# Optimization experiments

Hardware: AMD Instinct MI355X
Metric: run time of the kernel (lower is better)

## Reference

```python
import jax, jax.numpy as jnp
import numpy as np

B, N, D = 64, 512, 128  # graphs per batch, max nodes per graph, hidden_dim


def setup_inputs() -> dict:
    key = jax.random.key(0)
    ks = jax.random.split(key, 9)
    h1 = jax.random.normal(ks[0], (B, N, D), jnp.float32)
    h2 = jax.random.normal(ks[1], (B, N, D), jnp.float32)
    s = 1.0 / np.sqrt(D)
    Wk = jax.random.normal(ks[2], (D, D), jnp.float32) * s
    bk = jax.random.normal(ks[3], (D,), jnp.float32) * s
    Wq = jax.random.normal(ks[4], (D, D), jnp.float32) * s
    bq = jax.random.normal(ks[5], (D,), jnp.float32) * s
    t = jnp.asarray(np.sqrt(1.0 / D), jnp.float32)  # self.t = sqrt(1/hidden_dim)
    len1 = jax.random.randint(ks[6], (B,), 1, N + 1, jnp.int32)
    len2 = jax.random.randint(ks[7], (B,), 1, N + 1, jnp.int32)
    return {"h1": h1, "h2": h2, "Wk": Wk, "bk": bk, "Wq": Wq, "bq": bq,
            "t": t, "len1": len1, "len2": len2}


def reference(h1, h2, Wk, bk, Wq, bq, t, len1, len2):
    # valid-node masks for the ragged (padded) graphs
    pos = jnp.arange(N)
    m1 = pos[None, :] < len1[:, None]  # [B, N]
    m2 = pos[None, :] < len2[:, None]  # [B, N]

    # k = Linear(h), q = Linear(h)  (torch Linear: x @ W.T + b)
    k1 = jnp.einsum('bnd,ed->bne', h1, Wk) + bk
    k2 = jnp.einsum('bnd,ed->bne', h2, Wk) + bk
    q1 = jnp.einsum('bnd,ed->bne', h1, Wq) + bq
    q2 = jnp.einsum('bnd,ed->bne', h2, Wq) + bq

    NEG = jnp.asarray(-1e9, h1.dtype)

    # g1 nodes attend over g2 nodes; note values == keys (k2)
    s1 = jnp.einsum('bnd,bmd->bnm', q1, k2) * t           # [B, N1, N2]
    s1 = jnp.where(m2[:, None, :], s1, NEG)
    a1 = jax.nn.softmax(s1, axis=-1)
    o1 = jnp.einsum('bnm,bmd->bnd', a1, k2) * m1[:, :, None]

    # g2 nodes attend over g1 nodes; values == k1
    s2 = jnp.einsum('bnd,bmd->bnm', q2, k1) * t           # [B, N2, N1]
    s2 = jnp.where(m1[:, None, :], s2, NEG)
    a2 = jax.nn.softmax(s2, axis=-1)
    o2 = jnp.einsum('bnm,bmd->bnd', a2, k1) * m2[:, :, None]

    return o1, o2
```

## Files before the change

### kernel.cpp

```cpp
#include <hip/hip_runtime.h>

typedef __attribute__((ext_vector_type(8))) short bf16x8;
typedef __attribute__((ext_vector_type(4))) short s16x4;
typedef __attribute__((ext_vector_type(4))) float f32x4;
typedef __attribute__((ext_vector_type(4))) int   i32x4;

#define MFMA16 __builtin_amdgcn_mfma_f32_16x16x32_bf16

#define B_ 64
#define N_ 512
#define D_ 128
#define BUFB 16384

__device__ __forceinline__ unsigned short f2bf(float f) {
  unsigned u = __builtin_bit_cast(unsigned, f);
  u += 0x7fffu + ((u >> 16) & 1u);
  return (unsigned short)(u >> 16);
}
__device__ __forceinline__ int packbf2(float lo, float hi) {
  return (int)((unsigned)f2bf(lo) | ((unsigned)f2bf(hi) << 16));
}

__device__ __forceinline__ void gload_lds16(const void* g, void* l) {
  __builtin_amdgcn_global_load_lds((const __attribute__((address_space(1))) unsigned*)g,
                                   (__attribute__((address_space(3))) unsigned*)l, 16, 0, 0);
}

__global__ void prep_w(const float* __restrict__ Wk, const float* __restrict__ Wq,
                       const float* __restrict__ bq, const float* __restrict__ tptr,
                       short* __restrict__ wkb, short* __restrict__ wqb,
                       float* __restrict__ bqs) {
  const float sc = tptr[0] * 1.4426950408889634f;
  int i = blockIdx.x * 256 + threadIdx.x;
  if (i < D_ * D_) { wkb[i] = (short)f2bf(Wk[i]); wqb[i] = (short)f2bf(Wq[i] * sc); }
  if (i < D_) bqs[i] = bq[i] * sc;
}

__global__ __launch_bounds__(256, 2) void proj_kernel(
    const float* __restrict__ h1, const float* __restrict__ h2,
    const short* __restrict__ wkb, const short* __restrict__ wqb,
    const float* __restrict__ bk, const float* __restrict__ bqs,
    short* __restrict__ k1, short* __restrict__ k2,
    short* __restrict__ q1, short* __restrict__ q2,
    short* __restrict__ k1T, short* __restrict__ k2T) {
  const int wave = threadIdx.x >> 6, lane = threadIdx.x & 63;
  const int c = lane & 15, g = lane >> 4;
  const int rw = blockIdx.x * 128 + wave * 32;
  const int inp = rw >> 15;
  const int loc = rw & 32767;
  const int b = loc >> 9, n0 = loc & 511;
  const float* __restrict__ h = inp ? h2 : h1;
  short* __restrict__ kout = inp ? k2 : k1;
  short* __restrict__ qout = inp ? q2 : q1;
  short* __restrict__ kT   = inp ? k2T : k1T;

  bf16x8 xf[2][4];
#pragma unroll
  for (int mt = 0; mt < 2; ++mt) {
    const float* hr = h + (long)(loc + mt * 16 + c) * D_;
#pragma unroll
    for (int kk = 0; kk < 4; ++kk) {
      f32x4 lo = *(const f32x4*)(hr + kk * 32 + g * 8);
      f32x4 hi = *(const f32x4*)(hr + kk * 32 + g * 8 + 4);
      bf16x8 v;
      v[0] = (short)f2bf(lo[0]); v[1] = (short)f2bf(lo[1]);
      v[2] = (short)f2bf(lo[2]); v[3] = (short)f2bf(lo[3]);
      v[4] = (short)f2bf(hi[0]); v[5] = (short)f2bf(hi[1]);
      v[6] = (short)f2bf(hi[2]); v[7] = (short)f2bf(hi[3]);
      xf[mt][kk] = v;
    }
  }

#pragma unroll
  for (int et = 0; et < 8; ++et) {
    bf16x8 wkf[4], wqf[4];
    const short* wkr = wkb + (et * 16 + c) * D_;
    const short* wqr = wqb + (et * 16 + c) * D_;
#pragma unroll
    for (int kk = 0; kk < 4; ++kk) {
      wkf[kk] = *(const bf16x8*)(wkr + kk * 32 + g * 8);
      wqf[kk] = *(const bf16x8*)(wqr + kk * 32 + g * 8);
    }
    f32x4 ak[2], aq[2], at[2];
#pragma unroll
    for (int mt = 0; mt < 2; ++mt) {
      ak[mt] = (f32x4){0.f, 0.f, 0.f, 0.f};
      aq[mt] = (f32x4){0.f, 0.f, 0.f, 0.f};
      at[mt] = (f32x4){0.f, 0.f, 0.f, 0.f};
    }
#pragma unroll
    for (int kk = 0; kk < 4; ++kk) {
#pragma unroll
      for (int mt = 0; mt < 2; ++mt) {
        ak[mt] = MFMA16(wkf[kk], xf[mt][kk], ak[mt], 0, 0, 0);
        aq[mt] = MFMA16(wqf[kk], xf[mt][kk], aq[mt], 0, 0, 0);
        at[mt] = MFMA16(xf[mt][kk], wkf[kk], at[mt], 0, 0, 0);
      }
    }
    f32x4 bkv = *(const f32x4*)(bk + et * 16 + g * 4);
    f32x4 bqv = *(const f32x4*)(bqs + et * 16 + g * 4);
    float bks = bk[et * 16 + c];
#pragma unroll
    for (int mt = 0; mt < 2; ++mt) {
      s16x4 pk, pq, pt;
#pragma unroll
      for (int j = 0; j < 4; ++j) {
        pk[j] = (short)f2bf(ak[mt][j] + bkv[j]);
        pq[j] = (short)f2bf(aq[mt][j] + bqv[j]);
        pt[j] = (short)f2bf(at[mt][j] + bks);
      }
      long row = (long)(loc + mt * 16 + c);
      *(s16x4*)(kout + row * D_ + et * 16 + g * 4) = pk;
      *(s16x4*)(qout + row * D_ + et * 16 + g * 4) = pq;
      *(s16x4*)(kT + ((long)(b * D_ + et * 16 + c)) * N_ + n0 + mt * 16 + g * 4) = pt;
    }
  }
}

__global__ __launch_bounds__(128, 2) void attn_kernel(
    const short* __restrict__ k1, const short* __restrict__ k2,
    const short* __restrict__ q1, const short* __restrict__ q2,
    const short* __restrict__ k1T, const short* __restrict__ k2T,
    const int* __restrict__ len1, const int* __restrict__ len2,
    float* __restrict__ out) {
  __shared__ char smem[3 * BUFB];
  const int tid = threadIdx.x;
  const int wave = tid >> 6, lane = tid & 63;
  const int c = lane & 15, g = lane >> 4;
  const int wgid = blockIdx.x;
  const int qt = wgid >> 7;
  const int bd = wgid & 127;
  const int dir = bd >> 6, b = bd & 63;
  const short* __restrict__ qp = dir ? q2 : q1;
  const short* __restrict__ kp = dir ? k1 : k2;
  const short* __restrict__ vT = dir ? k1T : k2T;
  const int lk = dir ? len1[b] : len2[b];
  const int lq = dir ? len2[b] : len1[b];
  float* __restrict__ o = out + (long)dir * B_ * N_ * D_;

  if (qt * 64 >= lq) {
    f32x4 z = (f32x4){0.f, 0.f, 0.f, 0.f};
    f32x4* op = (f32x4*)(o + ((long)(b * N_ + qt * 64)) * D_);
#pragma unroll
    for (int i = 0; i < 16; ++i) op[i * 128 + tid] = z;
    return;
  }

  const int q0 = qt * 64 + wave * 32;
  const char* kbase = (const char*)(kp + (long)b * N_ * D_);
  const char* vbase = (const char*)(vT + (long)b * D_ * N_);

  auto stage = [&](int i, char* buf) {
#pragma unroll
    for (int j = 0; j < 4; ++j) {
      int L = j * 2048 + tid * 16;
      int row = L >> 8, off = L & 255;
      const char* gp = kbase + (i * 32 + row) * 256 + (off ^ ((row & 7) << 4));
      gload_lds16(gp, buf + j * 2048 + (wave << 10));
    }
#pragma unroll
    for (int j = 0; j < 4; ++j) {
      int L = j * 2048 + tid * 16;
      int row = L >> 6, off = L & 63;
      const char* gp = vbase + row * 1024 + i * 64 + (off ^ (((row >> 1) & 3) << 4));
      gload_lds16(gp, buf + 8192 + j * 2048 + (wave << 10));
    }
  };

  bf16x8 qf[2][4];
#pragma unroll
  for (int t = 0; t < 2; ++t) {
    const short* qrow = qp + ((long)(b * N_ + q0 + t * 16 + c)) * D_;
#pragma unroll
    for (int kk = 0; kk < 4; ++kk) qf[t][kk] = *(const bf16x8*)(qrow + kk * 32 + g * 8);
  }

  f32x4 oacc[2][8];
#pragma unroll
  for (int t = 0; t < 2; ++t)
#pragma unroll
    for (int dt = 0; dt < 8; ++dt) oacc[t][dt] = (f32x4){0.f, 0.f, 0.f, 0.f};
  float m[2] = {-3e38f, -3e38f};
  float l[2] = {0.f, 0.f};

  const int srcA = c + ((g & 1) << 5);
  const int srcB = srcA + 16;
  const bool lowhalf = (g < 2);

  const int nch = (lk + 31) >> 5;
  stage(0, smem);
  if (nch > 1) stage(1, smem + BUFB);
  int bi = 0;

  for (int ch = 0; ch < nch; ++ch) {
    if (ch + 1 < nch) { asm volatile("s_waitcnt vmcnt(8)" ::: "memory"); }
    else              { asm volatile("s_waitcnt vmcnt(0)" ::: "memory"); }
    __builtin_amdgcn_sched_barrier(0);
    __builtin_amdgcn_s_barrier();
    __builtin_amdgcn_sched_barrier(0);
    int si = bi + 2; if (si >= 3) si -= 3;
    if (ch + 2 < nch) stage(ch + 2, smem + BUFB * si);
    const char* buf = smem + BUFB * bi;
    bi = (bi + 1 == 3) ? 0 : bi + 1;
    const bool lastch = (ch == nch - 1);

    f32x4 sv[2][2];
    __builtin_amdgcn_s_setprio(1);
#pragma unroll
    for (int tl = 0; tl < 2; ++tl) {
      int r = tl * 16 + c;
      const char* base = buf + (r << 8);
      int sw = (r & 7) << 4;
      f32x4 a0 = (f32x4){0.f, 0.f, 0.f, 0.f};
      f32x4 a1 = (f32x4){0.f, 0.f, 0.f, 0.f};
#pragma unroll
      for (int kk = 0; kk < 4; ++kk) {
        bf16x8 kf = *(const bf16x8*)(base + ((kk * 64 + g * 16) ^ sw));
        a0 = MFMA16(kf, qf[0][kk], a0, 0, 0, 0);
        a1 = MFMA16(kf, qf[1][kk], a1, 0, 0, 0);
      }
      sv[0][tl] = a0; sv[1][tl] = a1;
    }
    __builtin_amdgcn_s_setprio(0);

    bf16x8 pf[2];
#pragma unroll
    for (int t = 0; t < 2; ++t) {
      float pmax = -3e38f;
      if (lastch) {
#pragma unroll
        for (int tl = 0; tl < 2; ++tl) {
          const int node = ch * 32 + tl * 16 + g * 4;
#pragma unroll
          for (int j = 0; j < 4; ++j) {
            float v = (node + j < lk) ? sv[t][tl][j] : -1e9f;
            sv[t][tl][j] = v;
            pmax = fmaxf(pmax, v);
          }
        }
      } else {
#pragma unroll
        for (int tl = 0; tl < 2; ++tl)
#pragma unroll
          for (int j = 0; j < 4; ++j) pmax = fmaxf(pmax, sv[t][tl][j]);
      }
      pmax = fmaxf(pmax, __shfl_xor(pmax, 16));
      pmax = fmaxf(pmax, __shfl_xor(pmax, 32));
      if (!__all(pmax - m[t] <= 11.5f)) {
        float newm = fmaxf(m[t], pmax);
        float sc = exp2f(m[t] - newm);
        m[t] = newm;
        l[t] *= sc;
#pragma unroll
        for (int dt = 0; dt < 8; ++dt)
#pragma unroll
          for (int j = 0; j < 4; ++j) oacc[t][dt][j] *= sc;
      }
      float sum = 0.f;
#pragma unroll
      for (int tl = 0; tl < 2; ++tl)
#pragma unroll
        for (int j = 0; j < 4; ++j) {
          float p = exp2f(sv[t][tl][j] - m[t]);
          sv[t][tl][j] = p;
          sum += p;
        }
      sum += __shfl_xor(sum, 16);
      sum += __shfl_xor(sum, 32);
      l[t] += sum;

      int a0 = packbf2(sv[t][0][0], sv[t][0][1]);
      int a1 = packbf2(sv[t][0][2], sv[t][0][3]);
      int b0 = packbf2(sv[t][1][0], sv[t][1][1]);
      int b1 = packbf2(sv[t][1][2], sv[t][1][3]);
      int xa0 = __shfl(a0, srcA), xb0 = __shfl(b0, srcA);
      int xa1 = __shfl(a1, srcA), xb1 = __shfl(b1, srcA);
      int ya0 = __shfl(a0, srcB), yb0 = __shfl(b0, srcB);
      int ya1 = __shfl(a1, srcB), yb1 = __shfl(b1, srcB);
      i32x4 ui;
      ui[0] = lowhalf ? xa0 : xb0;
      ui[1] = lowhalf ? xa1 : xb1;
      ui[2] = lowhalf ? ya0 : yb0;
      ui[3] = lowhalf ? ya1 : yb1;
      pf[t] = __builtin_bit_cast(bf16x8, ui);
    }

    __builtin_amdgcn_s_setprio(1);
#pragma unroll
    for (int dt = 0; dt < 8; ++dt) {
      int row = dt * 16 + c;
      const char* vb = buf + 8192 + row * 64;
      bf16x8 vt = *(const bf16x8*)(vb + ((g * 16) ^ (((row >> 1) & 3) << 4)));
      oacc[0][dt] = MFMA16(vt, pf[0], oacc[0][dt], 0, 0, 0);
      oacc[1][dt] = MFMA16(vt, pf[1], oacc[1][dt], 0, 0, 0);
    }
    __builtin_amdgcn_s_setprio(0);
  }

#pragma unroll
  for (int t = 0; t < 2; ++t) {
    const int qg = q0 + t * 16 + c;
    const bool valid = qg < lq;
    const float rinv = 1.0f / l[t];
    float* orow = o + ((long)(b * N_ + qg)) * D_;
#pragma unroll
    for (int dt = 0; dt < 8; ++dt) {
      f32x4 vo;
#pragma unroll
      for (int j = 0; j < 4; ++j) vo[j] = valid ? oacc[t][dt][j] * rinv : 0.0f;
      *(f32x4*)(orow + dt * 16 + g * 4) = vo;
    }
  }
}

extern "C" void kernel_launch(void* const* d_in, const int* in_sizes, int n_in,
                              void* d_out, int out_size, void* d_ws, size_t ws_size,
                              hipStream_t stream) {
  const float* h1 = (const float*)d_in[0];
  const float* h2 = (const float*)d_in[1];
  const float* Wk = (const float*)d_in[2];
  const float* bk = (const float*)d_in[3];
  const float* Wq = (const float*)d_in[4];
  const float* bq = (const float*)d_in[5];
  const float* t  = (const float*)d_in[6];
  const int* len1 = (const int*)d_in[7];
  const int* len2 = (const int*)d_in[8];

  char* ws = (char*)d_ws;
  const size_t SZ = (size_t)B_ * N_ * D_ * 2;
  short* k1  = (short*)(ws + 0 * SZ);
  short* k2  = (short*)(ws + 1 * SZ);
  short* q1  = (short*)(ws + 2 * SZ);
  short* q2  = (short*)(ws + 3 * SZ);
  short* k1T = (short*)(ws + 4 * SZ);
  short* k2T = (short*)(ws + 5 * SZ);
  short* wkb = (short*)(ws + 6 * SZ);
  short* wqb = (short*)(ws + 6 * SZ + D_ * D_ * 2);
  float* bqs = (float*)(ws + 6 * SZ + 2 * D_ * D_ * 2);

  prep_w<<<64, 256, 0, stream>>>(Wk, Wq, bq, t, wkb, wqb, bqs);
  proj_kernel<<<512, 256, 0, stream>>>(h1, h2, wkb, wqb, bk, bqs,
                                       k1, k2, q1, q2, k1T, k2T);
  attn_kernel<<<1024, 128, 0, stream>>>(k1, k2, q1, q2, k1T, k2T,
                                        len1, len2, (float*)d_out);
}
```

Baseline: 94.41 us.

## Replace LDS triple-buffered staging with direct register loads in attention kernel

The attention kernel no longer stages K and V^T tiles through shared memory with global_load_lds and barriers. Each wave now loads K fragments straight from global memory into registers, double-buffered across chunks, and loads V^T fragments per chunk. The grid changes to 256-thread blocks in which each wave handles its own 32-query tile, so there is no intra-block synchronisation. This removes barrier and LDS overhead but drops sharing of K/V between waves, relies on L2/L1 for reuse, and raises register pressure.

```diff
diff --git a/kernel.cpp b/kernel.cpp
--- a/kernel.cpp
+++ b/kernel.cpp
@@ -10,7 +10,6 @@
 #define B_ 64
 #define N_ 512
 #define D_ 128
-#define BUFB 16384
 
 __device__ __forceinline__ unsigned short f2bf(float f) {
   unsigned u = __builtin_bit_cast(unsigned, f);
@@ -19,11 +18,6 @@
 }
 __device__ __forceinline__ int packbf2(float lo, float hi) {
   return (int)((unsigned)f2bf(lo) | ((unsigned)f2bf(hi) << 16));
-}
-
-__device__ __forceinline__ void gload_lds16(const void* g, void* l) {
-  __builtin_amdgcn_global_load_lds((const __attribute__((address_space(1))) unsigned*)g,
-                                   (__attribute__((address_space(3))) unsigned*)l, 16, 0, 0);
 }
 
 __global__ void prep_w(const float* __restrict__ Wk, const float* __restrict__ Wq,
@@ -117,19 +111,17 @@
   }
 }
 
-__global__ __launch_bounds__(128, 2) void attn_kernel(
+__global__ __launch_bounds__(256) void attn_kernel(
     const short* __restrict__ k1, const short* __restrict__ k2,
     const short* __restrict__ q1, const short* __restrict__ q2,
     const short* __restrict__ k1T, const short* __restrict__ k2T,
     const int* __restrict__ len1, const int* __restrict__ len2,
     float* __restrict__ out) {
-  __shared__ char smem[3 * BUFB];
   const int tid = threadIdx.x;
   const int wave = tid >> 6, lane = tid & 63;
   const int c = lane & 15, g = lane >> 4;
-  const int wgid = blockIdx.x;
-  const int qt = wgid >> 7;
-  const int bd = wgid & 127;
+  const int bd = blockIdx.x & 127;
+  const int qt = ((blockIdx.x >> 7) << 2) + wave;
   const int dir = bd >> 6, b = bd & 63;
   const short* __restrict__ qp = dir ? q2 : q1;
   const short* __restrict__ kp = dir ? k1 : k2;
@@ -137,35 +129,18 @@
   const int lk = dir ? len1[b] : len2[b];
   const int lq = dir ? len2[b] : len1[b];
   float* __restrict__ o = out + (long)dir * B_ * N_ * D_;
-
-  if (qt * 64 >= lq) {
+  const int q0 = qt * 32;
+
+  if (q0 >= lq) {
     f32x4 z = (f32x4){0.f, 0.f, 0.f, 0.f};
-    f32x4* op = (f32x4*)(o + ((long)(b * N_ + qt * 64)) * D_);
-#pragma unroll
-    for (int i = 0; i < 16; ++i) op[i * 128 + tid] = z;
+    f32x4* op = (f32x4*)(o + ((long)(b * N_ + q0)) * D_);
+#pragma unroll
+    for (int i = 0; i < 16; ++i) op[i * 64 + lane] = z;
     return;
   }
 
-  const int q0 = qt * 64 + wave * 32;
   const char* kbase = (const char*)(kp + (long)b * N_ * D_);
   const char* vbase = (const char*)(vT + (long)b * D_ * N_);
-
-  auto stage = [&](int i, char* buf) {
-#pragma unroll
-    for (int j = 0; j < 4; ++j) {
-      int L = j * 2048 + tid * 16;
-      int row = L >> 8, off = L & 255;
-      const char* gp = kbase + (i * 32 + row) * 256 + (off ^ ((row & 7) << 4));
-      gload_lds16(gp, buf + j * 2048 + (wave << 10));
-    }
-#pragma unroll
-    for (int j = 0; j < 4; ++j) {
-      int L = j * 2048 + tid * 16;
-      int row = L >> 6, off = L & 63;
-      const char* gp = vbase + row * 1024 + i * 64 + (off ^ (((row >> 1) & 3) << 4));
-      gload_lds16(gp, buf + 8192 + j * 2048 + (wave << 10));
-    }
-  };
 
   bf16x8 qf[2][4];
 #pragma unroll
@@ -186,43 +161,40 @@
   const int srcA = c + ((g & 1) << 5);
   const int srcB = srcA + 16;
   const bool lowhalf = (g < 2);
-
   const int nch = (lk + 31) >> 5;
-  stage(0, smem);
-  if (nch > 1) stage(1, smem + BUFB);
-  int bi = 0;
-
-  for (int ch = 0; ch < nch; ++ch) {
-    if (ch + 1 < nch) { asm volatile("s_waitcnt vmcnt(8)" ::: "memory"); }
-    else              { asm volatile("s_waitcnt vmcnt(0)" ::: "memory"); }
-    __builtin_amdgcn_sched_barrier(0);
-    __builtin_amdgcn_s_barrier();
-    __builtin_amdgcn_sched_barrier(0);
-    int si = bi + 2; if (si >= 3) si -= 3;
-    if (ch + 2 < nch) stage(ch + 2, smem + BUFB * si);
-    const char* buf = smem + BUFB * bi;
-    bi = (bi + 1 == 3) ? 0 : bi + 1;
-    const bool lastch = (ch == nch - 1);
+
+  auto loadk = [&](bf16x8 (&kf)[2][4], int ch) {
+#pragma unroll
+    for (int tl = 0; tl < 2; ++tl) {
+      const char* base = kbase + (ch * 32 + tl * 16 + c) * 256;
+#pragma unroll
+      for (int kk = 0; kk < 4; ++kk)
+        kf[tl][kk] = *(const bf16x8*)(base + kk * 64 + g * 16);
+    }
+  };
+
+  auto body = [&](bf16x8 (&kfc)[2][4], bf16x8 (&kfn)[2][4], int ch) {
+    bf16x8 vt[8];
+#pragma unroll
+    for (int dt = 0; dt < 8; ++dt)
+      vt[dt] = *(const bf16x8*)(vbase + (dt * 16 + c) * 1024 + ch * 64 + g * 16);
 
     f32x4 sv[2][2];
-    __builtin_amdgcn_s_setprio(1);
 #pragma unroll
     for (int tl = 0; tl < 2; ++tl) {
-      int r = tl * 16 + c;
-      const char* base = buf + (r << 8);
-      int sw = (r & 7) << 4;
       f32x4 a0 = (f32x4){0.f, 0.f, 0.f, 0.f};
       f32x4 a1 = (f32x4){0.f, 0.f, 0.f, 0.f};
 #pragma unroll
       for (int kk = 0; kk < 4; ++kk) {
-        bf16x8 kf = *(const bf16x8*)(base + ((kk * 64 + g * 16) ^ sw));
-        a0 = MFMA16(kf, qf[0][kk], a0, 0, 0, 0);
-        a1 = MFMA16(kf, qf[1][kk], a1, 0, 0, 0);
+        a0 = MFMA16(kfc[tl][kk], qf[0][kk], a0, 0, 0, 0);
+        a1 = MFMA16(kfc[tl][kk], qf[1][kk], a1, 0, 0, 0);
       }
       sv[0][tl] = a0; sv[1][tl] = a1;
     }
-    __builtin_amdgcn_s_setprio(0);
-
+
+    if (ch + 1 < nch) loadk(kfn, ch + 1);
+
+    const bool lastch = (ch == nch - 1);
     bf16x8 pf[2];
 #pragma unroll
     for (int t = 0; t < 2; ++t) {
@@ -285,16 +257,21 @@
       pf[t] = __builtin_bit_cast(bf16x8, ui);
     }
 
-    __builtin_amdgcn_s_setprio(1);
 #pragma unroll
     for (int dt = 0; dt < 8; ++dt) {
-      int row = dt * 16 + c;
-      const char* vb = buf + 8192 + row * 64;
-      bf16x8 vt = *(const bf16x8*)(vb + ((g * 16) ^ (((row >> 1) & 3) << 4)));
-      oacc[0][dt] = MFMA16(vt, pf[0], oacc[0][dt], 0, 0, 0);
-      oacc[1][dt] = MFMA16(vt, pf[1], oacc[1][dt], 0, 0, 0);
-    }
-    __builtin_amdgcn_s_setprio(0);
+      oacc[0][dt] = MFMA16(vt[dt], pf[0], oacc[0][dt], 0, 0, 0);
+      oacc[1][dt] = MFMA16(vt[dt], pf[1], oacc[1][dt], 0, 0, 0);
+    }
+  };
+
+  bf16x8 kfA[2][4], kfB[2][4];
+  loadk(kfA, 0);
+  int ch = 0;
+  while (true) {
+    body(kfA, kfB, ch);
+    if (++ch >= nch) break;
+    body(kfB, kfA, ch);
+    if (++ch >= nch) break;
   }
 
 #pragma unroll
@@ -341,6 +318,6 @@
   prep_w<<<64, 256, 0, stream>>>(Wk, Wq, bq, t, wkb, wqb, bqs);
   proj_kernel<<<512, 256, 0, stream>>>(h1, h2, wkb, wqb, bk, bqs,
                                        k1, k2, q1, q2, k1T, k2T);
-  attn_kernel<<<1024, 128, 0, stream>>>(k1, k2, q1, q2, k1T, k2T,
-                                        len1, len2, (float*)d_out);
-}
+  attn_kernel<<<512, 256, 0, stream>>>(k1, k2, q1, q2, k1T, k2T,
+                                       len1, len2, (float*)d_out);
+}
```

Measured after the change: 99.79 us. 1.06x slower.
